# Performance work log

Hardware: AMD Instinct MI355X
Metric: run time of the kernel (lower is better)

## Reference

```python
import jax, jax.numpy as jnp
import numpy as np

DIM = 1536
HEADS = 12
HD = DIM // HEADS  # 128
EPS = 1e-6
SINK_SIZE = 1          # frames
MAX_ATTN = 1920        # tokens (sliding window)


def setup_inputs() -> dict:
    key = jax.random.key(0)
    ks = jax.random.split(key, 10)
    B = 1
    F, H, W = 8, 16, 24
    L = F * H * W  # 3072
    s = 0.02
    inp = {
        "x": jax.random.normal(ks[0], (B, L, DIM), jnp.float32),
        "seq_lens": jnp.array([L], jnp.int32),
        "grid_sizes": jnp.array([[F, H, W]], jnp.int32),
        "freqs": jax.random.normal(ks[1], (1024, HD // 2, 2), jnp.float32),
        "wq": jax.random.normal(ks[2], (DIM, DIM), jnp.float32) * s,
        "bq": jnp.zeros((DIM,), jnp.float32),
        "wk": jax.random.normal(ks[3], (DIM, DIM), jnp.float32) * s,
        "bk": jnp.zeros((DIM,), jnp.float32),
        "wv": jax.random.normal(ks[4], (DIM, DIM), jnp.float32) * s,
        "bv": jnp.zeros((DIM,), jnp.float32),
        "wo": jax.random.normal(ks[5], (DIM, DIM), jnp.float32) * s,
        "bo": jnp.zeros((DIM,), jnp.float32),
        "nq_w": jnp.ones((DIM,), jnp.float32),
        "nk_w": jnp.ones((DIM,), jnp.float32),
    }
    return inp


def _rmsnorm(x, w):
    # WanRMSNorm: x * rsqrt(mean(x^2) + eps) * weight
    return x * jax.lax.rsqrt(jnp.mean(x * x, axis=-1, keepdims=True) + EPS) * w


def _rope(x, F, H, W, fc):
    # x: [B, L, n, d]; fc: complex [1024, d//2]
    B, L, n, d = x.shape
    c = d // 2
    c1 = c - 2 * (c // 3)  # temporal split
    c2 = c // 3
    f0, f1, f2 = fc[:, :c1], fc[:, c1:c1 + c2], fc[:, c1 + c2:]
    fr = jnp.concatenate([
        jnp.broadcast_to(f0[:F, None, None, :], (F, H, W, c1)),
        jnp.broadcast_to(f1[None, :H, None, :], (F, H, W, c2)),
        jnp.broadcast_to(f2[None, None, :W, :], (F, H, W, c2)),
    ], axis=-1).reshape(L, 1, c)  # [L, 1, c]
    xp = x.reshape(B, L, n, c, 2)
    xc = jax.lax.complex(xp[..., 0], xp[..., 1])  # [B, L, n, c]
    xr = xc * fr[None]
    return jnp.stack([jnp.real(xr), jnp.imag(xr)], axis=-1).reshape(B, L, n, d)


def reference(x, seq_lens, grid_sizes, freqs, wq, bq, wk, bk, wv, bv, wo, bo, nq_w, nk_w):
    B, L, _ = x.shape
    gs = np.asarray(grid_sizes)[0]
    F, H, W = int(gs[0]), int(gs[1]), int(gs[2])
    fs = H * W  # frame_seqlen
    sink = SINK_SIZE * fs

    q = _rmsnorm(x @ wq.T + bq, nq_w).reshape(B, L, HEADS, HD)
    k = _rmsnorm(x @ wk.T + bk, nk_w).reshape(B, L, HEADS, HD)
    v = (x @ wv.T + bv).reshape(B, L, HEADS, HD)

    fc = jax.lax.complex(freqs[..., 0], freqs[..., 1])  # [1024, HD//2]
    q = _rope(q, F, H, W, fc)
    k = _rope(k, F, H, W, fc)

    # sink + windowed frame-causal block mask (flex_attention block_mask)
    idx = jnp.arange(L)
    qf = idx // fs
    kf = idx // fs
    mask = (kf[None, :] <= qf[:, None]) & (
        (idx[None, :] < sink) | (idx[None, :] >= (qf[:, None] + 1) * fs - MAX_ATTN)
    )  # [L, L]

    scale = 1.0 / np.float32(np.sqrt(HD))
    scores = jnp.einsum('bqnd,bknd->bnqk', q, k) * scale
    scores = jnp.where(mask[None, None], scores, jnp.float32(-1e30))
    attn = jax.nn.softmax(scores, axis=-1)
    out = jnp.einsum('bnqk,bknd->bqnd', attn, v).reshape(B, L, DIM)
    return out @ wo.T + bo
```

## Files before the change

kernel.cpp:

```cpp
#include <hip/hip_runtime.h>
#include <stdint.h>

#define DIMC 1536
#define LTOK 3072
#define HEADS 12
#define HD 128
#define FS 384
#define MAXATTN 1920
#define HTOK 1152
#define NHT 1920

typedef __attribute__((ext_vector_type(4))) float f32x4;
typedef __attribute__((ext_vector_type(8))) short bf16x8;
typedef __attribute__((ext_vector_type(4))) unsigned int u32x4;

__device__ __forceinline__ unsigned short f2bf(float f) {
  union { float f; unsigned int u; } c; c.f = f;
  unsigned int u = c.u + 0x7fffu + ((c.u >> 16) & 1u);
  return (unsigned short)(u >> 16);
}
__device__ __forceinline__ float bf2f(unsigned short s) {
  union { unsigned int u; float f; } c; c.u = (unsigned int)s << 16; return c.f;
}

__device__ __forceinline__ void dma16(const void* g, void* l) {
  __builtin_amdgcn_global_load_lds(
      (const __attribute__((address_space(1))) unsigned int*)g,
      (__attribute__((address_space(3))) unsigned int*)l, 16, 0, 0);
}

__device__ __forceinline__ int vperm4(int G) {
  return (((G >> 3) & 1) << 3) | (((G >> 1) & 1) << 2) | ((G & 1) << 1) | ((G >> 2) & 1);
}

__global__ __launch_bounds__(256)
void cvt_all_k(const float* __restrict__ x, const float* __restrict__ wq,
               const float* __restrict__ wk, const float* __restrict__ wv,
               const float* __restrict__ wo,
               unsigned short* __restrict__ xb, unsigned short* __restrict__ wqb,
               unsigned short* __restrict__ wkb, unsigned short* __restrict__ wvb,
               unsigned short* __restrict__ wob)
{
  const int i = blockIdx.x * 256 + threadIdx.x;
  const int n0 = LTOK * DIMC / 4;
  const int nw = DIMC * DIMC / 4;
  const float* src; unsigned short* dst; int off;
  if (i < n0) { src = x; dst = xb; off = i; }
  else {
    int j = i - n0; int w = j / nw; off = j - w * nw;
    src = (w == 0) ? wq : (w == 1) ? wk : (w == 2) ? wv : wo;
    dst = (w == 0) ? wqb : (w == 1) ? wkb : (w == 2) ? wvb : wob;
  }
  float4 f = ((const float4*)src)[off];
  uint2 o;
  o.x = (unsigned int)f2bf(f.x) | ((unsigned int)f2bf(f.y) << 16);
  o.y = (unsigned int)f2bf(f.z) | ((unsigned int)f2bf(f.w) << 16);
  ((uint2*)dst)[off] = o;
}

__global__ __launch_bounds__(256)
void gemm_qkv(const unsigned short* __restrict__ A,
              const unsigned short* __restrict__ B0,
              const unsigned short* __restrict__ B1,
              const unsigned short* __restrict__ B2,
              const float* __restrict__ bias0,
              const float* __restrict__ bias1,
              const float* __restrict__ bias2,
              unsigned short* __restrict__ o0, unsigned short* __restrict__ o1,
              unsigned short* __restrict__ vt)
{
  const int z = blockIdx.z;
  const unsigned short* Bw = (z == 0) ? B0 : (z == 1) ? B1 : B2;
  const float* bias = (z == 0) ? bias0 : (z == 1) ? bias1 : bias2;

  __shared__ __align__(16) unsigned short lA[128 * 64];
  __shared__ __align__(16) unsigned short lB[128 * 64];

  const int tid = threadIdx.x;
  const int wave = tid >> 6;
  const int lane = tid & 63;
  const int m0 = blockIdx.y * 128;
  const int n0 = blockIdx.x * 128;
  const int wm = (wave >> 1) * 64;
  const int wn = (wave & 1) * 64;

  f32x4 acc[4][4] = {};

  const int srow = tid >> 3;
  const int scol = ((tid & 7) ^ (srow & 7)) * 8;
  const unsigned short* ga = A  + (size_t)(m0 + srow) * DIMC + scol;
  const unsigned short* gb = Bw + (size_t)(n0 + srow) * DIMC + scol;
  unsigned short* la = lA + tid * 8;
  unsigned short* lb = lB + tid * 8;

  const int fr = lane & 15;
  const int g = lane >> 4;
  const int fx = fr & 7;

  for (int k0 = 0; k0 < DIMC; k0 += 64) {
    dma16(ga + k0,                     la);
    dma16(ga + k0 + (size_t)32 * DIMC, la + 2048);
    dma16(ga + k0 + (size_t)64 * DIMC, la + 4096);
    dma16(ga + k0 + (size_t)96 * DIMC, la + 6144);
    dma16(gb + k0,                     lb);
    dma16(gb + k0 + (size_t)32 * DIMC, lb + 2048);
    dma16(gb + k0 + (size_t)64 * DIMC, lb + 4096);
    dma16(gb + k0 + (size_t)96 * DIMC, lb + 6144);
    __syncthreads();

#pragma unroll
    for (int kk = 0; kk < 2; ++kk) {
      const int cx = ((kk * 4 + g) ^ fx) * 8;
      bf16x8 af[4], bf[4];
#pragma unroll
      for (int i = 0; i < 4; ++i)
        af[i] = *(const bf16x8*)&lA[(wm + i * 16 + fr) * 64 + cx];
#pragma unroll
      for (int j = 0; j < 4; ++j)
        bf[j] = *(const bf16x8*)&lB[(wn + j * 16 + fr) * 64 + cx];
#pragma unroll
      for (int i = 0; i < 4; ++i)
#pragma unroll
        for (int j = 0; j < 4; ++j)
          acc[i][j] = __builtin_amdgcn_mfma_f32_16x16x32_bf16(af[i], bf[j], acc[i][j], 0, 0, 0);
    }
    __syncthreads();
  }

  const int col = lane & 15;
  const int rb = (lane >> 4) * 4;
  if (z < 2) {
    unsigned short* outp = z ? o1 : o0;
#pragma unroll
    for (int j = 0; j < 4; ++j) {
      const int gn = n0 + wn + j * 16 + col;
      const float bv = bias[gn];
#pragma unroll
      for (int i = 0; i < 4; ++i)
#pragma unroll
        for (int r = 0; r < 4; ++r) {
          const int gm = m0 + wm + i * 16 + rb + r;
          outp[(size_t)gm * DIMC + gn] = f2bf(acc[i][j][r] + bv);
        }
    }
  } else {
#pragma unroll
    for (int j = 0; j < 4; ++j) {
      const int gn = n0 + wn + j * 16 + col;
      const float bv = bias[gn];
#pragma unroll
      for (int i = 0; i < 4; ++i) {
        const int base = wm + i * 16 + rb;
        const int tile = base & ~63;
        const int toka = m0 + tile + vperm4((base & 63) >> 2) * 4;
        uint2 pk;
        pk.x = (unsigned int)f2bf(acc[i][j][0] + bv) |
               ((unsigned int)f2bf(acc[i][j][1] + bv) << 16);
        pk.y = (unsigned int)f2bf(acc[i][j][2] + bv) |
               ((unsigned int)f2bf(acc[i][j][3] + bv) << 16);
        *(uint2*)(vt + (size_t)gn * LTOK + toka) = pk;
      }
    }
  }
}

__global__ __launch_bounds__(256)
void gemm_wo(const unsigned short* __restrict__ A,
             const unsigned short* __restrict__ Bw,
             const float* __restrict__ bias,
             float* __restrict__ outp)
{
  __shared__ __align__(16) unsigned short lA[64 * 64];
  __shared__ __align__(16) unsigned short lB[128 * 64];

  const int tid = threadIdx.x;
  const int wave = tid >> 6;
  const int lane = tid & 63;
  const int m0 = blockIdx.y * 64;
  const int n0 = blockIdx.x * 128;
  const int wm = (wave >> 1) * 32;
  const int wn = (wave & 1) * 64;

  f32x4 acc[2][4] = {};

  const int srow = tid >> 3;
  const int scol = ((tid & 7) ^ (srow & 7)) * 8;
  const unsigned short* ga = A  + (size_t)(m0 + srow) * DIMC + scol;
  const unsigned short* gb = Bw + (size_t)(n0 + srow) * DIMC + scol;
  unsigned short* la = lA + tid * 8;
  unsigned short* lb = lB + tid * 8;

  const int fr = lane & 15;
  const int g = lane >> 4;
  const int fx = fr & 7;

  for (int k0 = 0; k0 < DIMC; k0 += 64) {
    dma16(ga + k0,                     la);
    dma16(ga + k0 + (size_t)32 * DIMC, la + 2048);
    dma16(gb + k0,                     lb);
    dma16(gb + k0 + (size_t)32 * DIMC, lb + 2048);
    dma16(gb + k0 + (size_t)64 * DIMC, lb + 4096);
    dma16(gb + k0 + (size_t)96 * DIMC, lb + 6144);
    __syncthreads();

#pragma unroll
    for (int kk = 0; kk < 2; ++kk) {
      const int cx = ((kk * 4 + g) ^ fx) * 8;
      bf16x8 af[2], bf[4];
#pragma unroll
      for (int i = 0; i < 2; ++i)
        af[i] = *(const bf16x8*)&lA[(wm + i * 16 + fr) * 64 + cx];
#pragma unroll
      for (int j = 0; j < 4; ++j)
        bf[j] = *(const bf16x8*)&lB[(wn + j * 16 + fr) * 64 + cx];
#pragma unroll
      for (int i = 0; i < 2; ++i)
#pragma unroll
        for (int j = 0; j < 4; ++j)
          acc[i][j] = __builtin_amdgcn_mfma_f32_16x16x32_bf16(af[i], bf[j], acc[i][j], 0, 0, 0);
    }
    __syncthreads();
  }

  const int col = lane & 15;
  const int rb = (lane >> 4) * 4;
#pragma unroll
  for (int j = 0; j < 4; ++j) {
    const int gn = n0 + wn + j * 16 + col;
    const float bv = bias[gn];
#pragma unroll
    for (int i = 0; i < 2; ++i)
#pragma unroll
      for (int r = 0; r < 4; ++r) {
        const int gm = m0 + wm + i * 16 + rb + r;
        outp[(size_t)gm * DIMC + gn] = acc[i][j][r] + bv;
      }
  }
}

__global__ __launch_bounds__(256)
void post_qkv_k(unsigned short* __restrict__ q, unsigned short* __restrict__ k,
                const float* __restrict__ nqw, const float* __restrict__ nkw,
                const float* __restrict__ freqs)
{
  const int bx = blockIdx.x;
  const int tid = threadIdx.x;
  const int which = bx >= LTOK;
  const int tok = bx - which * LTOK;
  unsigned short* row = (which ? k : q) + (size_t)tok * DIMC;
  const float* nw = which ? nkw : nqw;
  const float sc = which ? 1.f : (0.08838834764831845f * 1.4426950408889634f);
  const int base = tid * 6;

  float vv[6];
  float ss = 0.f;
#pragma unroll
  for (int j = 0; j < 6; ++j) {
    vv[j] = bf2f(row[base + j]);
    ss += vv[j] * vv[j];
  }
#pragma unroll
  for (int off = 1; off < 64; off <<= 1) ss += __shfl_xor(ss, off);
  __shared__ float wsum[4];
  if ((tid & 63) == 0) wsum[tid >> 6] = ss;
  __syncthreads();
  const float total = wsum[0] + wsum[1] + wsum[2] + wsum[3];
  const float rms = rsqrtf(total * (1.f / DIMC) + 1e-6f);

  const int f = tok / FS;
  const int rem = tok - f * FS;
  const int h = rem / 24;
  const int w = rem - h * 24;

#pragma unroll
  for (int pp = 0; pp < 3; ++pp) {
    const int P = (base >> 1) + pp;
    const int p = P & 63;
    const int t = (p < 22) ? f : ((p < 43) ? h : w);
    const float fre = freqs[t * 128 + p * 2];
    const float fim = freqs[t * 128 + p * 2 + 1];
    const float e = vv[2 * pp]     * rms * nw[base + 2 * pp];
    const float o = vv[2 * pp + 1] * rms * nw[base + 2 * pp + 1];
    row[base + 2 * pp]     = f2bf((e * fre - o * fim) * sc);
    row[base + 2 * pp + 1] = f2bf((e * fim + o * fre) * sc);
  }
}

#define KBUF (64 * 128)
#define VBUF (128 * 64)
__global__ __launch_bounds__(256, 2)
void attn_flash(const unsigned short* __restrict__ q,
                const unsigned short* __restrict__ k,
                const unsigned short* __restrict__ vt,
                unsigned short* __restrict__ ab,
                float* __restrict__ Opart,
                float* __restrict__ mlbuf)
{
  const int bid = blockIdx.x;
  int qb, head, chunk, nchunks;
  if (bid < 360) { const int hb = bid >> 1; qb = 23 - hb / 12; head = hb % 12; chunk = bid & 1; nchunks = 2; }
  else           { const int lb = bid - 360; qb = 8 - lb / 12; head = lb % 12; chunk = 0; nchunks = 1; }

  const int q0 = qb * 128;
  const int qf = qb / 3;
  const int kend = (qf + 1) * FS;
  const int s2 = kend - MAXATTN;
  const bool two = (s2 > FS);
  const int nt1 = (two ? FS : kend) >> 6;
  const int nt  = nt1 + (two ? (MAXATTN >> 6) : 0);
  const int half = nt / nchunks;
  const int tstart = chunk * half, tend = tstart + half;

  const int tid = threadIdx.x;
  const int wave = tid >> 6, lane = tid & 63;
  const int col = lane & 15;
  const int g = lane >> 4;
  const int g4 = g * 4;

  __shared__ __align__(16) unsigned short Kl[2 * KBUF];
  __shared__ __align__(16) unsigned short Vtl[2 * VBUF];

  bf16x8 qfA[4], qfB[4];
  {
    const unsigned short* qr0 = q + (size_t)(q0 + wave * 32 + col) * DIMC + head * HD;
#pragma unroll
    for (int kk = 0; kk < 4; ++kk) {
      qfA[kk] = *(const bf16x8*)(qr0 + kk * 32 + g * 8);
      qfB[kk] = *(const bf16x8*)(qr0 + (size_t)16 * DIMC + kk * 32 + g * 8);
    }
  }

  f32x4 o0[8] = {}, o1[8] = {};
  float m0 = -3.0e38f, l0 = 0.f, m1 = -3.0e38f, l1 = 0.f;

  const int krow = tid >> 4;
  const int kc8  = ((tid & 15) ^ krow) * 8;
  const unsigned short* kg = k + (size_t)krow * DIMC + head * HD + kc8;
  const int vrow = tid >> 3;
  const int vc8  = ((tid & 7) ^ (vrow & 7)) * 8;
  const unsigned short* vg = vt + ((size_t)head * HD + vrow) * LTOK + vc8;
  unsigned short* kl = Kl + tid * 8;
  unsigned short* vl = Vtl + tid * 8;

  {
    const int kb = (tstart < nt1) ? tstart * 64 : s2 + (tstart - nt1) * 64;
    const unsigned short* kp = kg + (size_t)kb * DIMC;
    dma16(kp,                     kl);
    dma16(kp + (size_t)16 * DIMC, kl + 16 * 128);
    dma16(kp + (size_t)32 * DIMC, kl + 32 * 128);
    dma16(kp + (size_t)48 * DIMC, kl + 48 * 128);
    const unsigned short* vp = vg + kb;
    dma16(vp,                     vl);
    dma16(vp + (size_t)32 * LTOK, vl + 32 * 64);
    dma16(vp + (size_t)64 * LTOK, vl + 64 * 64);
    dma16(vp + (size_t)96 * LTOK, vl + 96 * 64);
  }

  for (int t = tstart; t < tend; ++t) {
    const int kcur = ((t - tstart) & 1) * KBUF;
    const int vcur = ((t - tstart) & 1) * VBUF;
    __syncthreads();

    if (t + 1 < tend) {
      const int kb = (t + 1 < nt1) ? (t + 1) * 64 : s2 + (t + 1 - nt1) * 64;
      const int knxt = KBUF - kcur, vnxt = VBUF - vcur;
      const unsigned short* kp = kg + (size_t)kb * DIMC;
      dma16(kp,                     kl + knxt);
      dma16(kp + (size_t)16 * DIMC, kl + knxt + 16 * 128);
      dma16(kp + (size_t)32 * DIMC, kl + knxt + 32 * 128);
      dma16(kp + (size_t)48 * DIMC, kl + knxt + 48 * 128);
      const unsigned short* vp = vg + kb;
      dma16(vp,                     vl + vnxt);
      dma16(vp + (size_t)32 * LTOK, vl + vnxt + 32 * 64);
      dma16(vp + (size_t)64 * LTOK, vl + vnxt + 64 * 64);
      dma16(vp + (size_t)96 * LTOK, vl + vnxt + 96 * 64);
    }

    f32x4 sA[4] = {}, sB[4] = {};
#pragma unroll
    for (int kt = 0; kt < 4; ++kt) {
      const unsigned short* kr = &Kl[kcur + (kt * 16 + col) * 128];
#pragma unroll
      for (int kk = 0; kk < 4; ++kk) {
        bf16x8 kfr = *(const bf16x8*)(kr + ((kk * 4 + g) ^ col) * 8);
        sA[kt] = __builtin_amdgcn_mfma_f32_16x16x32_bf16(kfr, qfA[kk], sA[kt], 0, 0, 0);
        sB[kt] = __builtin_amdgcn_mfma_f32_16x16x32_bf16(kfr, qfB[kk], sB[kt], 0, 0, 0);
      }
    }

    unsigned int A0, A1, A2, A3, A4, A5, A6, A7;
    float alA;
    {
      float mx = sA[0][0];
#pragma unroll
      for (int kt = 0; kt < 4; ++kt)
#pragma unroll
        for (int r = 0; r < 4; ++r) mx = fmaxf(mx, sA[kt][r]);
      mx = fmaxf(mx, __shfl_xor(mx, 16));
      mx = fmaxf(mx, __shfl_xor(mx, 32));
      const float mn = fmaxf(m0, mx);
      alA = exp2f(m0 - mn);
      m0 = mn;
      float rs = 0.f;
#define PKA(KT, PA, PB)                                        \
      {                                                        \
        const unsigned short p0 = f2bf(exp2f(sA[KT][0] - mn)); \
        const unsigned short p1 = f2bf(exp2f(sA[KT][1] - mn)); \
        const unsigned short p2 = f2bf(exp2f(sA[KT][2] - mn)); \
        const unsigned short p3 = f2bf(exp2f(sA[KT][3] - mn)); \
        rs += bf2f(p0) + bf2f(p1) + bf2f(p2) + bf2f(p3);       \
        PA = (unsigned int)p0 | ((unsigned int)p1 << 16);      \
        PB = (unsigned int)p2 | ((unsigned int)p3 << 16);      \
      }
      PKA(0, A0, A1) PKA(1, A2, A3) PKA(2, A4, A5) PKA(3, A6, A7)
#undef PKA
      rs += __shfl_xor(rs, 16);
      rs += __shfl_xor(rs, 32);
      l0 = l0 * alA + rs;
    }
    unsigned int B0, B1, B2, B3, B4, B5, B6, B7;
    float alB;
    {
      float mx = sB[0][0];
#pragma unroll
      for (int kt = 0; kt < 4; ++kt)
#pragma unroll
        for (int r = 0; r < 4; ++r) mx = fmaxf(mx, sB[kt][r]);
      mx = fmaxf(mx, __shfl_xor(mx, 16));
      mx = fmaxf(mx, __shfl_xor(mx, 32));
      const float mn = fmaxf(m1, mx);
      alB = exp2f(m1 - mn);
      m1 = mn;
      float rs = 0.f;
#define PKB(KT, PA, PB)                                        \
      {                                                        \
        const unsigned short p0 = f2bf(exp2f(sB[KT][0] - mn)); \
        const unsigned short p1 = f2bf(exp2f(sB[KT][1] - mn)); \
        const unsigned short p2 = f2bf(exp2f(sB[KT][2] - mn)); \
        const unsigned short p3 = f2bf(exp2f(sB[KT][3] - mn)); \
        rs += bf2f(p0) + bf2f(p1) + bf2f(p2) + bf2f(p3);       \
        PA = (unsigned int)p0 | ((unsigned int)p1 << 16);      \
        PB = (unsigned int)p2 | ((unsigned int)p3 << 16);      \
      }
      PKB(0, B0, B1) PKB(1, B2, B3) PKB(2, B4, B5) PKB(3, B6, B7)
#undef PKB
      rs += __shfl_xor(rs, 16);
      rs += __shfl_xor(rs, 32);
      l1 = l1 * alB + rs;
    }

#pragma unroll
    for (int dt = 0; dt < 8; ++dt) { o0[dt] *= alA; o1[dt] *= alB; }

    u32x4 tA0, tA1, tB0, tB1;
    tA0[0] = A0; tA0[1] = A1; tA0[2] = A2; tA0[3] = A3;
    tA1[0] = A4; tA1[1] = A5; tA1[2] = A6; tA1[3] = A7;
    tB0[0] = B0; tB0[1] = B1; tB0[2] = B2; tB0[3] = B3;
    tB1[0] = B4; tB1[1] = B5; tB1[2] = B6; tB1[3] = B7;
    const bf16x8 pfA0 = __builtin_bit_cast(bf16x8, tA0);
    const bf16x8 pfA1 = __builtin_bit_cast(bf16x8, tA1);
    const bf16x8 pfB0 = __builtin_bit_cast(bf16x8, tB0);
    const bf16x8 pfB1 = __builtin_bit_cast(bf16x8, tB1);

    const int vx0 = (g ^ (col & 7)) * 8;
    const int vx1 = ((4 + g) ^ (col & 7)) * 8;
#pragma unroll
    for (int dt = 0; dt < 8; ++dt) {
      const unsigned short* vr = &Vtl[vcur + (dt * 16 + col) * 64];
      bf16x8 vf0 = *(const bf16x8*)(vr + vx0);
      o0[dt] = __builtin_amdgcn_mfma_f32_16x16x32_bf16(vf0, pfA0, o0[dt], 0, 0, 0);
      o1[dt] = __builtin_amdgcn_mfma_f32_16x16x32_bf16(vf0, pfB0, o1[dt], 0, 0, 0);
      bf16x8 vf1 = *(const bf16x8*)(vr + vx1);
      o0[dt] = __builtin_amdgcn_mfma_f32_16x16x32_bf16(vf1, pfA1, o0[dt], 0, 0, 0);
      o1[dt] = __builtin_amdgcn_mfma_f32_16x16x32_bf16(vf1, pfB1, o1[dt], 0, 0, 0);
    }
  }

  const int qrow0 = q0 + wave * 32 + col;
  if (nchunks == 1) {
    const float i0 = 1.f / l0, i1 = 1.f / l1;
    unsigned short* or0 = ab + (size_t)qrow0 * DIMC + head * HD;
    unsigned short* or1 = or0 + (size_t)16 * DIMC;
#pragma unroll
    for (int dt = 0; dt < 8; ++dt) {
      uint2 pk;
      pk.x = (unsigned int)f2bf(o0[dt][0] * i0) | ((unsigned int)f2bf(o0[dt][1] * i0) << 16);
      pk.y = (unsigned int)f2bf(o0[dt][2] * i0) | ((unsigned int)f2bf(o0[dt][3] * i0) << 16);
      *(uint2*)(or0 + dt * 16 + g4) = pk;
      pk.x = (unsigned int)f2bf(o1[dt][0] * i1) | ((unsigned int)f2bf(o1[dt][1] * i1) << 16);
      pk.y = (unsigned int)f2bf(o1[dt][2] * i1) | ((unsigned int)f2bf(o1[dt][3] * i1) << 16);
      *(uint2*)(or1 + dt * 16 + g4) = pk;
    }
  } else {
    const int tokp0 = qrow0 - HTOK;
    float* ob0 = Opart + ((size_t)(chunk * NHT + tokp0) * HEADS + head) * HD;
    float* ob1 = Opart + ((size_t)(chunk * NHT + tokp0 + 16) * HEADS + head) * HD;
#pragma unroll
    for (int dt = 0; dt < 8; ++dt) {
      *(f32x4*)(ob0 + dt * 16 + g4) = o0[dt];
      *(f32x4*)(ob1 + dt * 16 + g4) = o1[dt];
    }
    if (lane < 16) {
      float* mlp0 = mlbuf + 2 * ((size_t)(chunk * NHT + tokp0) * HEADS + head);
      float* mlp1 = mlbuf + 2 * ((size_t)(chunk * NHT + tokp0 + 16) * HEADS + head);
      mlp0[0] = m0; mlp0[1] = l0;
      mlp1[0] = m1; mlp1[1] = l1;
    }
  }
}

__global__ __launch_bounds__(384)
void merge_k(const float* __restrict__ Opart, const float* __restrict__ mlbuf,
             unsigned short* __restrict__ ab)
{
  const int tokp = blockIdx.x;
  const int tid = threadIdx.x;
  const int e = tid * 4;
  const int head = e >> 7;
  const size_t r0 = (size_t)tokp * DIMC + e;
  float4 o0 = *(const float4*)(Opart + r0);
  float4 o1 = *(const float4*)(Opart + (size_t)NHT * DIMC + r0);
  const float* ml0 = mlbuf + 2 * ((size_t)tokp * HEADS + head);
  const float* ml1 = mlbuf + 2 * ((size_t)(NHT + tokp) * HEADS + head);
  const float m0 = ml0[0], l0 = ml0[1], m1 = ml1[0], l1 = ml1[1];
  const float mm = fmaxf(m0, m1);
  const float a0 = exp2f(m0 - mm), a1 = exp2f(m1 - mm);
  const float inv = 1.f / (l0 * a0 + l1 * a1);
  uint2 pk;
  pk.x = (unsigned int)f2bf((o0.x * a0 + o1.x * a1) * inv) |
         ((unsigned int)f2bf((o0.y * a0 + o1.y * a1) * inv) << 16);
  pk.y = (unsigned int)f2bf((o0.z * a0 + o1.z * a1) * inv) |
         ((unsigned int)f2bf((o0.w * a0 + o1.w * a1) * inv) << 16);
  *(uint2*)(ab + (size_t)(HTOK + tokp) * DIMC + e) = pk;
}

extern "C" void kernel_launch(void* const* d_in, const int* in_sizes, int n_in,
                              void* d_out, int out_size, void* d_ws, size_t ws_size,
                              hipStream_t stream)
{
  (void)in_sizes; (void)n_in; (void)out_size; (void)ws_size;
  const float* x     = (const float*)d_in[0];
  const float* freqs = (const float*)d_in[3];
  const float* wq    = (const float*)d_in[4];
  const float* bq    = (const float*)d_in[5];
  const float* wk    = (const float*)d_in[6];
  const float* bk    = (const float*)d_in[7];
  const float* wv    = (const float*)d_in[8];
  const float* bv    = (const float*)d_in[9];
  const float* wo    = (const float*)d_in[10];
  const float* bo    = (const float*)d_in[11];
  const float* nqw   = (const float*)d_in[12];
  const float* nkw   = (const float*)d_in[13];

  char* ws = (char*)d_ws;
  size_t off = 0;
  auto take = [&](size_t bytes) -> void* {
    void* p = ws + off; off += (bytes + 255) & ~(size_t)255; return p;
  };
  unsigned short* wob = (unsigned short*)take((size_t)DIMC * DIMC * 2);
  unsigned short* qb  = (unsigned short*)take((size_t)LTOK * DIMC * 2);
  unsigned short* kb  = (unsigned short*)take((size_t)LTOK * DIMC * 2);
  unsigned short* vb  = (unsigned short*)take((size_t)LTOK * DIMC * 2);
  unsigned short* ab  = (unsigned short*)take((size_t)LTOK * DIMC * 2);
  unsigned short* vtb = (unsigned short*)take((size_t)LTOK * DIMC * 2);
  unsigned short* xb  = (unsigned short*)take((size_t)LTOK * DIMC * 2);
  unsigned short* wqb = (unsigned short*)take((size_t)DIMC * DIMC * 2);
  unsigned short* wkb = (unsigned short*)take((size_t)DIMC * DIMC * 2);
  unsigned short* wvb = (unsigned short*)take((size_t)DIMC * DIMC * 2);
  float* mlb = (float*)take((size_t)2 * NHT * HEADS * 2 * sizeof(float));
  float* Opart = (float*)xb;
  (void)vb;

  cvt_all_k<<<dim3(13824), dim3(256), 0, stream>>>(x, wq, wk, wv, wo,
                                                   xb, wqb, wkb, wvb, wob);

  gemm_qkv<<<dim3(DIMC / 128, LTOK / 128, 3), dim3(256), 0, stream>>>(
      xb, wqb, wkb, wvb, bq, bk, bv, qb, kb, vtb);

  post_qkv_k<<<dim3(2 * LTOK), dim3(256), 0, stream>>>(qb, kb, nqw, nkw, freqs);

  attn_flash<<<dim3(468), dim3(256), 0, stream>>>(qb, kb, vtb, ab, Opart, mlb);
  merge_k<<<dim3(NHT), dim3(384), 0, stream>>>(Opart, mlb, ab);

  gemm_wo<<<dim3(DIMC / 128, LTOK / 64), dim3(256), 0, stream>>>(
      ab, wob, bo, (float*)d_out);
}
```

Measured before the change: 283.9 us.

## Split attention block into 8 waves of 16 query rows with MFMA priority hints

The flash-attention kernel moves from 4 waves each handling 32 query rows to 8 waves (512 threads) each handling 16 rows. This halves per-wave register state and doubles the waves cooperating on each K/V tile load. It also wraps the MFMA loops in s_setprio so matrix work gets issue priority over softmax and load work. In exchange, K/V shared-memory reads are amortised over fewer rows per wave, and each wave now runs its own softmax reduction.

```diff
diff --git a/kernel.cpp b/kernel.cpp
--- a/kernel.cpp
+++ b/kernel.cpp
@@ -288,7 +288,7 @@
 
 #define KBUF (64 * 128)
 #define VBUF (128 * 64)
-__global__ __launch_bounds__(256, 2)
+__global__ __launch_bounds__(512, 4)
 void attn_flash(const unsigned short* __restrict__ q,
                 const unsigned short* __restrict__ k,
                 const unsigned short* __restrict__ vt,
@@ -320,21 +320,19 @@
   __shared__ __align__(16) unsigned short Kl[2 * KBUF];
   __shared__ __align__(16) unsigned short Vtl[2 * VBUF];
 
-  bf16x8 qfA[4], qfB[4];
+  bf16x8 qfA[4];
   {
-    const unsigned short* qr0 = q + (size_t)(q0 + wave * 32 + col) * DIMC + head * HD;
-#pragma unroll
-    for (int kk = 0; kk < 4; ++kk) {
+    const unsigned short* qr0 = q + (size_t)(q0 + wave * 16 + col) * DIMC + head * HD;
+#pragma unroll
+    for (int kk = 0; kk < 4; ++kk)
       qfA[kk] = *(const bf16x8*)(qr0 + kk * 32 + g * 8);
-      qfB[kk] = *(const bf16x8*)(qr0 + (size_t)16 * DIMC + kk * 32 + g * 8);
-    }
-  }
-
-  f32x4 o0[8] = {}, o1[8] = {};
-  float m0 = -3.0e38f, l0 = 0.f, m1 = -3.0e38f, l1 = 0.f;
+  }
+
+  f32x4 o0[8] = {};
+  float m0 = -3.0e38f, l0 = 0.f;
 
   const int krow = tid >> 4;
-  const int kc8  = ((tid & 15) ^ krow) * 8;
+  const int kc8  = ((tid & 15) ^ (krow & 15)) * 8;
   const unsigned short* kg = k + (size_t)krow * DIMC + head * HD + kc8;
   const int vrow = tid >> 3;
   const int vc8  = ((tid & 7) ^ (vrow & 7)) * 8;
@@ -346,14 +344,10 @@
     const int kb = (tstart < nt1) ? tstart * 64 : s2 + (tstart - nt1) * 64;
     const unsigned short* kp = kg + (size_t)kb * DIMC;
     dma16(kp,                     kl);
-    dma16(kp + (size_t)16 * DIMC, kl + 16 * 128);
     dma16(kp + (size_t)32 * DIMC, kl + 32 * 128);
-    dma16(kp + (size_t)48 * DIMC, kl + 48 * 128);
     const unsigned short* vp = vg + kb;
     dma16(vp,                     vl);
-    dma16(vp + (size_t)32 * LTOK, vl + 32 * 64);
     dma16(vp + (size_t)64 * LTOK, vl + 64 * 64);
-    dma16(vp + (size_t)96 * LTOK, vl + 96 * 64);
   }
 
   for (int t = tstart; t < tend; ++t) {
@@ -366,17 +360,14 @@
       const int knxt = KBUF - kcur, vnxt = VBUF - vcur;
       const unsigned short* kp = kg + (size_t)kb * DIMC;
       dma16(kp,                     kl + knxt);
-      dma16(kp + (size_t)16 * DIMC, kl + knxt + 16 * 128);
       dma16(kp + (size_t)32 * DIMC, kl + knxt + 32 * 128);
-      dma16(kp + (size_t)48 * DIMC, kl + knxt + 48 * 128);
       const unsigned short* vp = vg + kb;
       dma16(vp,                     vl + vnxt);
-      dma16(vp + (size_t)32 * LTOK, vl + vnxt + 32 * 64);
       dma16(vp + (size_t)64 * LTOK, vl + vnxt + 64 * 64);
-      dma16(vp + (size_t)96 * LTOK, vl + vnxt + 96 * 64);
-    }
-
-    f32x4 sA[4] = {}, sB[4] = {};
+    }
+
+    f32x4 sA[4] = {};
+    __builtin_amdgcn_s_setprio(1);
 #pragma unroll
     for (int kt = 0; kt < 4; ++kt) {
       const unsigned short* kr = &Kl[kcur + (kt * 16 + col) * 128];
@@ -384,9 +375,9 @@
       for (int kk = 0; kk < 4; ++kk) {
         bf16x8 kfr = *(const bf16x8*)(kr + ((kk * 4 + g) ^ col) * 8);
         sA[kt] = __builtin_amdgcn_mfma_f32_16x16x32_bf16(kfr, qfA[kk], sA[kt], 0, 0, 0);
-        sB[kt] = __builtin_amdgcn_mfma_f32_16x16x32_bf16(kfr, qfB[kk], sB[kt], 0, 0, 0);
       }
     }
+    __builtin_amdgcn_s_setprio(0);
 
     unsigned int A0, A1, A2, A3, A4, A5, A6, A7;
     float alA;
@@ -418,93 +409,50 @@
       rs += __shfl_xor(rs, 32);
       l0 = l0 * alA + rs;
     }
-    unsigned int B0, B1, B2, B3, B4, B5, B6, B7;
-    float alB;
-    {
-      float mx = sB[0][0];
-#pragma unroll
-      for (int kt = 0; kt < 4; ++kt)
-#pragma unroll
-        for (int r = 0; r < 4; ++r) mx = fmaxf(mx, sB[kt][r]);
-      mx = fmaxf(mx, __shfl_xor(mx, 16));
-      mx = fmaxf(mx, __shfl_xor(mx, 32));
-      const float mn = fmaxf(m1, mx);
-      alB = exp2f(m1 - mn);
-      m1 = mn;
-      float rs = 0.f;
-#define PKB(KT, PA, PB)                                        \
-      {                                                        \
-        const unsigned short p0 = f2bf(exp2f(sB[KT][0] - mn)); \
-        const unsigned short p1 = f2bf(exp2f(sB[KT][1] - mn)); \
-        const unsigned short p2 = f2bf(exp2f(sB[KT][2] - mn)); \
-        const unsigned short p3 = f2bf(exp2f(sB[KT][3] - mn)); \
-        rs += bf2f(p0) + bf2f(p1) + bf2f(p2) + bf2f(p3);       \
-        PA = (unsigned int)p0 | ((unsigned int)p1 << 16);      \
-        PB = (unsigned int)p2 | ((unsigned int)p3 << 16);      \
-      }
-      PKB(0, B0, B1) PKB(1, B2, B3) PKB(2, B4, B5) PKB(3, B6, B7)
-#undef PKB
-      rs += __shfl_xor(rs, 16);
-      rs += __shfl_xor(rs, 32);
-      l1 = l1 * alB + rs;
-    }
-
-#pragma unroll
-    for (int dt = 0; dt < 8; ++dt) { o0[dt] *= alA; o1[dt] *= alB; }
-
-    u32x4 tA0, tA1, tB0, tB1;
+
+#pragma unroll
+    for (int dt = 0; dt < 8; ++dt) o0[dt] *= alA;
+
+    u32x4 tA0, tA1;
     tA0[0] = A0; tA0[1] = A1; tA0[2] = A2; tA0[3] = A3;
     tA1[0] = A4; tA1[1] = A5; tA1[2] = A6; tA1[3] = A7;
-    tB0[0] = B0; tB0[1] = B1; tB0[2] = B2; tB0[3] = B3;
-    tB1[0] = B4; tB1[1] = B5; tB1[2] = B6; tB1[3] = B7;
     const bf16x8 pfA0 = __builtin_bit_cast(bf16x8, tA0);
     const bf16x8 pfA1 = __builtin_bit_cast(bf16x8, tA1);
-    const bf16x8 pfB0 = __builtin_bit_cast(bf16x8, tB0);
-    const bf16x8 pfB1 = __builtin_bit_cast(bf16x8, tB1);
 
     const int vx0 = (g ^ (col & 7)) * 8;
     const int vx1 = ((4 + g) ^ (col & 7)) * 8;
+    __builtin_amdgcn_s_setprio(1);
 #pragma unroll
     for (int dt = 0; dt < 8; ++dt) {
       const unsigned short* vr = &Vtl[vcur + (dt * 16 + col) * 64];
       bf16x8 vf0 = *(const bf16x8*)(vr + vx0);
       o0[dt] = __builtin_amdgcn_mfma_f32_16x16x32_bf16(vf0, pfA0, o0[dt], 0, 0, 0);
-      o1[dt] = __builtin_amdgcn_mfma_f32_16x16x32_bf16(vf0, pfB0, o1[dt], 0, 0, 0);
       bf16x8 vf1 = *(const bf16x8*)(vr + vx1);
       o0[dt] = __builtin_amdgcn_mfma_f32_16x16x32_bf16(vf1, pfA1, o0[dt], 0, 0, 0);
-      o1[dt] = __builtin_amdgcn_mfma_f32_16x16x32_bf16(vf1, pfB1, o1[dt], 0, 0, 0);
-    }
-  }
-
-  const int qrow0 = q0 + wave * 32 + col;
+    }
+    __builtin_amdgcn_s_setprio(0);
+  }
+
+  const int qrow0 = q0 + wave * 16 + col;
   if (nchunks == 1) {
-    const float i0 = 1.f / l0, i1 = 1.f / l1;
+    const float i0 = 1.f / l0;
     unsigned short* or0 = ab + (size_t)qrow0 * DIMC + head * HD;
-    unsigned short* or1 = or0 + (size_t)16 * DIMC;
 #pragma unroll
     for (int dt = 0; dt < 8; ++dt) {
       uint2 pk;
       pk.x = (unsigned int)f2bf(o0[dt][0] * i0) | ((unsigned int)f2bf(o0[dt][1] * i0) << 16);
       pk.y = (unsigned int)f2bf(o0[dt][2] * i0) | ((unsigned int)f2bf(o0[dt][3] * i0) << 16);
       *(uint2*)(or0 + dt * 16 + g4) = pk;
-      pk.x = (unsigned int)f2bf(o1[dt][0] * i1) | ((unsigned int)f2bf(o1[dt][1] * i1) << 16);
-      pk.y = (unsigned int)f2bf(o1[dt][2] * i1) | ((unsigned int)f2bf(o1[dt][3] * i1) << 16);
-      *(uint2*)(or1 + dt * 16 + g4) = pk;
     }
   } else {
     const int tokp0 = qrow0 - HTOK;
     float* ob0 = Opart + ((size_t)(chunk * NHT + tokp0) * HEADS + head) * HD;
-    float* ob1 = Opart + ((size_t)(chunk * NHT + tokp0 + 16) * HEADS + head) * HD;
-#pragma unroll
-    for (int dt = 0; dt < 8; ++dt) {
+#pragma unroll
+    for (int dt = 0; dt < 8; ++dt)
       *(f32x4*)(ob0 + dt * 16 + g4) = o0[dt];
-      *(f32x4*)(ob1 + dt * 16 + g4) = o1[dt];
-    }
     if (lane < 16) {
       float* mlp0 = mlbuf + 2 * ((size_t)(chunk * NHT + tokp0) * HEADS + head);
-      float* mlp1 = mlbuf + 2 * ((size_t)(chunk * NHT + tokp0 + 16) * HEADS + head);
       mlp0[0] = m0; mlp0[1] = l0;
-      mlp1[0] = m1; mlp1[1] = l1;
     }
   }
 }
@@ -579,7 +527,7 @@
 
   post_qkv_k<<<dim3(2 * LTOK), dim3(256), 0, stream>>>(qb, kb, nqw, nkw, freqs);
 
-  attn_flash<<<dim3(468), dim3(256), 0, stream>>>(qb, kb, vtb, ab, Opart, mlb);
+  attn_flash<<<dim3(468), dim3(512), 0, stream>>>(qb, kb, vtb, ab, Opart, mlb);
   merge_k<<<dim3(NHT), dim3(384), 0, stream>>>(Opart, mlb, ab);
 
   gemm_wo<<<dim3(DIMC / 128, LTOK / 64), dim3(256), 0, stream>>>(
```

Result: no change. 281.9 us (-0.7%).
